# Optimization experiments

Hardware: AMD Instinct MI355X
Metric: run time of the kernel (lower is better)

The kernel has to match this reference:

```python
import jax, jax.numpy as jnp
import numpy as np

B, N, C, H = 4, 1024, 1024, 16
D = C // H                      # head_dim = 64
FFH = int(int(C * 4.0) * 2 / 3) # 2730
EPS = 1e-6


def rmsnorm(x, w):
    return w * (x * jax.lax.rsqrt(jnp.mean(x * x, axis=-1, keepdims=True) + EPS))


def setup_inputs() -> dict:
    key = jax.random.key(0)
    ks = jax.random.split(key, 12)
    s = 0.02
    return {
        "x": jax.random.normal(ks[0], (B, N, C), jnp.float32),
        "c": jax.random.normal(ks[1], (B, C), jnp.float32),
        "norm1_w": jnp.ones((C,), jnp.float32),
        "norm2_w": jnp.ones((C,), jnp.float32),
        "qkv_w": jax.random.normal(ks[2], (3 * C, C), jnp.float32) * s,
        "qkv_b": jnp.zeros((3 * C,), jnp.float32),
        "q_norm_w": jnp.ones((D,), jnp.float32),
        "k_norm_w": jnp.ones((D,), jnp.float32),
        "proj_w": jax.random.normal(ks[3], (C, C), jnp.float32) * s,
        "proj_b": jnp.zeros((C,), jnp.float32),
        "w12_w": jax.random.normal(ks[4], (2 * FFH, C), jnp.float32) * s,
        "w12_b": jnp.zeros((2 * FFH,), jnp.float32),
        "w3_w": jax.random.normal(ks[5], (C, FFH), jnp.float32) * s,
        "w3_b": jnp.zeros((C,), jnp.float32),
        "ada_w": jax.random.normal(ks[6], (6 * C, C), jnp.float32) * s,
        "ada_b": jnp.zeros((6 * C,), jnp.float32),
    }


def modulate(x, shift, scale):
    return x * (1.0 + scale[:, None, :]) + shift[:, None, :]


def attention(x, qkv_w, qkv_b, q_norm_w, k_norm_w, proj_w, proj_b):
    qkv = x @ qkv_w.T + qkv_b                       # (B,N,3C)
    qkv = qkv.reshape(B, N, 3, H, D)
    q, k, v = qkv[:, :, 0], qkv[:, :, 1], qkv[:, :, 2]   # (B,N,H,D)
    q = jnp.transpose(q, (0, 2, 1, 3))              # (B,H,N,D)
    k = jnp.transpose(k, (0, 2, 1, 3))
    v = jnp.transpose(v, (0, 2, 1, 3))
    q = rmsnorm(q, q_norm_w)
    k = rmsnorm(k, k_norm_w)
    attn = jnp.einsum("bhnd,bhmd->bhnm", q, k) / jnp.sqrt(jnp.float32(D))
    attn = jax.nn.softmax(attn, axis=-1)
    out = jnp.einsum("bhnm,bhmd->bhnd", attn, v)
    out = jnp.transpose(out, (0, 2, 1, 3)).reshape(B, N, C)
    return out @ proj_w.T + proj_b


def swiglu(x, w12_w, w12_b, w3_w, w3_b):
    x12 = x @ w12_w.T + w12_b                       # (B,N,2*FFH)
    x1, x2 = x12[..., :FFH], x12[..., FFH:]
    h = jax.nn.silu(x1) * x2
    return h @ w3_w.T + w3_b


def reference(x, c, norm1_w, norm2_w, qkv_w, qkv_b, q_norm_w, k_norm_w,
              proj_w, proj_b, w12_w, w12_b, w3_w, w3_b, ada_w, ada_b):
    ada = jax.nn.silu(c) @ ada_w.T + ada_b          # (B,6C)
    s1, g1, b1, s2, g2, b2 = jnp.split(ada, 6, axis=-1)
    a = attention(modulate(rmsnorm(x, norm1_w), s1, g1),
                  qkv_w, qkv_b, q_norm_w, k_norm_w, proj_w, proj_b)
    x = x + b1[:, None, :] * a
    m = swiglu(modulate(rmsnorm(x, norm2_w), s2, g2), w12_w, w12_b, w3_w, w3_b)
    x = x + b2[:, None, :] * m
    return x
```

## Files before the change

kernel.cpp:

```cpp
#include <hip/hip_runtime.h>

typedef short s16x8 __attribute__((ext_vector_type(8)));
typedef short s16x4 __attribute__((ext_vector_type(4)));
typedef float f32x4 __attribute__((ext_vector_type(4)));

#define B_   4
#define N_   1024
#define C_   1024
#define H_   16
#define D_   64
#define FFH_ 2730
#define FFP_ 2752

__device__ __forceinline__ short f2bf(float f) {
  unsigned u = __float_as_uint(f);
  u += 0x7fff + ((u >> 16) & 1);
  return (short)(unsigned short)(u >> 16);
}
__device__ __forceinline__ float bf2f(short s) {
  return __uint_as_float(((unsigned)(unsigned short)s) << 16);
}
__device__ __forceinline__ float silu(float x) { return x / (1.f + __expf(-x)); }

__device__ __forceinline__ void gload16(const void* g, void* l) {
  __builtin_amdgcn_global_load_lds(
      (const __attribute__((address_space(1))) unsigned*)g,
      (__attribute__((address_space(3))) unsigned*)l, 16, 0, 0);
}

__global__ void cvt3(const float* __restrict__ s0, short* __restrict__ d0, const int n0,
                     const float* __restrict__ s1, short* __restrict__ d1, const int n1,
                     const float* __restrict__ s2, short* __restrict__ d2, const int n2) {
  const int tot = n0 + n1 + n2;
  for (int i = blockIdx.x * 256 + threadIdx.x; i < tot; i += gridDim.x * 256) {
    const float* s; short* d; int j = i;
    if (j < n0)            { s = s0; d = d0; }
    else if ((j -= n0) < n1) { s = s1; d = d1; }
    else                   { j -= n1; s = s2; d = d2; }
    const float4 v = ((const float4*)s)[j];
    s16x4 o;
    o[0] = f2bf(v.x); o[1] = f2bf(v.y); o[2] = f2bf(v.z); o[3] = f2bf(v.w);
    *(s16x4*)(d + (size_t)j * 4) = o;
  }
}

__global__ void cvt_w3(const float* __restrict__ s, short* __restrict__ d) {
  const int col = blockIdx.x * 256 + threadIdx.x;
  const int row = blockIdx.y;
  if (col < FFP_)
    d[(size_t)row * FFP_ + col] = (col < FFH_) ? f2bf(s[(size_t)row * FFH_ + col]) : (short)0;
}

__global__ void ada_gemm(const float* __restrict__ c, const float* __restrict__ aw,
                         const float* __restrict__ ab, float* __restrict__ ada) {
  const int j = blockIdx.x;
  const int l = threadIdx.x;
  float acc[4] = {0.f, 0.f, 0.f, 0.f};
  const float4* wr = (const float4*)(aw + (size_t)j * 1024);
  #pragma unroll
  for (int p = 0; p < 4; ++p) {
    const float4 wv = wr[p * 64 + l];
    #pragma unroll
    for (int b = 0; b < 4; ++b) {
      const float4 cv = ((const float4*)(c + b * 1024))[p * 64 + l];
      acc[b] += silu(cv.x) * wv.x + silu(cv.y) * wv.y + silu(cv.z) * wv.z + silu(cv.w) * wv.w;
    }
  }
  #pragma unroll
  for (int b = 0; b < 4; ++b) {
    float a = acc[b];
    #pragma unroll
    for (int m = 1; m < 64; m <<= 1) a += __shfl_xor(a, m);
    if (l == 0) ada[b * 6144 + j] = a + ab[j];
  }
}

__global__ void rmsmod(const float* __restrict__ x, const float* __restrict__ wn,
                       const float* __restrict__ ada, const int sOff, const int gOff,
                       short* __restrict__ out) {
  const int row = blockIdx.x;
  const int b = row >> 10;
  const int t = threadIdx.x;
  const float4 v = ((const float4*)(x + (size_t)row * 1024))[t];
  float ss = v.x * v.x + v.y * v.y + v.z * v.z + v.w * v.w;
  #pragma unroll
  for (int m = 1; m < 64; m <<= 1) ss += __shfl_xor(ss, m);
  __shared__ float red[4];
  if ((t & 63) == 0) red[t >> 6] = ss;
  __syncthreads();
  const float rs = rsqrtf((red[0] + red[1] + red[2] + red[3]) * (1.f / 1024.f) + 1e-6f);
  const int j = t * 4;
  const float* sp = ada + b * 6144 + sOff + j;
  const float* gp = ada + b * 6144 + gOff + j;
  s16x4 o;
  o[0] = f2bf(v.x * rs * wn[j + 0] * (1.f + gp[0]) + sp[0]);
  o[1] = f2bf(v.y * rs * wn[j + 1] * (1.f + gp[1]) + sp[1]);
  o[2] = f2bf(v.z * rs * wn[j + 2] * (1.f + gp[2]) + sp[2]);
  o[3] = f2bf(v.w * rs * wn[j + 3] * (1.f + gp[3]) + sp[3]);
  *(s16x4*)(out + (size_t)row * 1024 + j) = o;
}

__global__ void rmsmod_b(const short* __restrict__ x, const float* __restrict__ wn,
                         const float* __restrict__ ada, const int sOff, const int gOff,
                         short* __restrict__ out) {
  const int row = blockIdx.x;
  const int b = row >> 10;
  const int t = threadIdx.x;
  const s16x4 vb = *(const s16x4*)(x + (size_t)row * 1024 + t * 4);
  const float v0 = bf2f(vb[0]), v1 = bf2f(vb[1]), v2 = bf2f(vb[2]), v3 = bf2f(vb[3]);
  float ss = v0 * v0 + v1 * v1 + v2 * v2 + v3 * v3;
  #pragma unroll
  for (int m = 1; m < 64; m <<= 1) ss += __shfl_xor(ss, m);
  __shared__ float red[4];
  if ((t & 63) == 0) red[t >> 6] = ss;
  __syncthreads();
  const float rs = rsqrtf((red[0] + red[1] + red[2] + red[3]) * (1.f / 1024.f) + 1e-6f);
  const int j = t * 4;
  const float* sp = ada + b * 6144 + sOff + j;
  const float* gp = ada + b * 6144 + gOff + j;
  s16x4 o;
  o[0] = f2bf(v0 * rs * wn[j + 0] * (1.f + gp[0]) + sp[0]);
  o[1] = f2bf(v1 * rs * wn[j + 1] * (1.f + gp[1]) + sp[1]);
  o[2] = f2bf(v2 * rs * wn[j + 2] * (1.f + gp[2]) + sp[2]);
  o[3] = f2bf(v3 * rs * wn[j + 3] * (1.f + gp[3]) + sp[3]);
  *(s16x4*)(out + (size_t)row * 1024 + j) = o;
}

__launch_bounds__(256, 2)
__global__ void gemm_qkv(const short* __restrict__ A, const short* __restrict__ Bt,
                         const float* __restrict__ bias,
                         short* __restrict__ qbO, short* __restrict__ kbO,
                         short* __restrict__ vrO,
                         const float* __restrict__ qnw, const float* __restrict__ knw) {
  __shared__ short As[128 * 64];
  __shared__ short Bs[128 * 64];
  const int t = threadIdx.x;
  const int l = t & 63;
  const int w = t >> 6;
  const int wr = (w >> 1) * 64, wc = (w & 1) * 64;
  const int K = 1024;

  const int nwg = gridDim.x * gridDim.y;
  int lin = blockIdx.y * gridDim.x + blockIdx.x;
  lin = (lin & 7) * (nwg >> 3) + (lin >> 3);
  const int m0 = (lin / gridDim.x) * 128;
  const int n0 = (lin % gridDim.x) * 128;

  f32x4 acc[4][4];
  const f32x4 z4 = {0.f, 0.f, 0.f, 0.f};
  #pragma unroll
  for (int i = 0; i < 4; ++i)
    #pragma unroll
    for (int j = 0; j < 4; ++j) acc[i][j] = z4;

  const int lr = l >> 3;
  const int lc = (l & 7) ^ lr;
  const short* gAs = A + (size_t)(m0 + w * 32 + lr) * K + lc * 8;
  const short* gBs = Bt + (size_t)(n0 + w * 32 + lr) * K + lc * 8;
  short* lA = As + (w * 32) * 64;
  short* lB = Bs + (w * 32) * 64;

  for (int kt = 0; kt < 16; ++kt) {
    if (kt) __syncthreads();
    const int ko = kt * 64;
    #pragma unroll
    for (int p = 0; p < 4; ++p) {
      gload16(gAs + (size_t)p * 8 * K + ko, lA + p * 8 * 64);
      gload16(gBs + (size_t)p * 8 * K + ko, lB + p * 8 * 64);
    }
    __syncthreads();
    #pragma unroll
    for (int kk = 0; kk < 2; ++kk) {
      const int c16 = kk * 4 + (l >> 4);
      s16x8 af[4], bfr[4];
      #pragma unroll
      for (int mf = 0; mf < 4; ++mf) {
        const int r = wr + mf * 16 + (l & 15);
        af[mf] = *(const s16x8*)&As[r * 64 + ((c16 ^ (r & 7)) << 3)];
      }
      #pragma unroll
      for (int nf = 0; nf < 4; ++nf) {
        const int r = wc + nf * 16 + (l & 15);
        bfr[nf] = *(const s16x8*)&Bs[r * 64 + ((c16 ^ (r & 7)) << 3)];
      }
      __builtin_amdgcn_s_setprio(1);
      #pragma unroll
      for (int mf = 0; mf < 4; ++mf)
        #pragma unroll
        for (int nf = 0; nf < 4; ++nf)
          acc[mf][nf] = __builtin_amdgcn_mfma_f32_16x16x32_bf16(af[mf], bfr[nf], acc[mf][nf], 0, 0, 0);
      __builtin_amdgcn_s_setprio(0);
    }
  }

  const int colB = n0 + wc;
  const int sec = colB >> 10;
  const int hh = (colB >> 6) & 15;
  if (sec < 2) {
    short* dst = sec ? kbO : qbO;
    const float* nw = sec ? knw : qnw;
    const float scl = sec ? 1.f : 0.125f;
    #pragma unroll
    for (int mf = 0; mf < 4; ++mf) {
      #pragma unroll
      for (int i = 0; i < 4; ++i) {
        const int row = m0 + wr + mf * 16 + ((l >> 4) << 2) + i;
        float vv[4];
        float ss = 0.f;
        #pragma unroll
        for (int nf = 0; nf < 4; ++nf) {
          vv[nf] = acc[mf][nf][i] + bias[colB + nf * 16 + (l & 15)];
          ss += vv[nf] * vv[nf];
        }
        ss += __shfl_xor(ss, 1); ss += __shfl_xor(ss, 2);
        ss += __shfl_xor(ss, 4); ss += __shfl_xor(ss, 8);
        const float rs = rsqrtf(ss * (1.f / 64.f) + 1e-6f) * scl;
        const int bb = row >> 10, nn = row & 1023;
        #pragma unroll
        for (int nf = 0; nf < 4; ++nf) {
          const int d = nf * 16 + (l & 15);
          dst[((size_t)(bb * 16 + hh) * 1024 + nn) * 64 + d] = f2bf(vv[nf] * rs * nw[d]);
        }
      }
    }
  } else {
    #pragma unroll
    for (int mf = 0; mf < 4; ++mf)
      #pragma unroll
      for (int nf = 0; nf < 4; ++nf) {
        const int col = colB + nf * 16 + (l & 15);
        const float bsv = bias[col];
        #pragma unroll
        for (int i = 0; i < 4; ++i) {
          const int row = m0 + wr + mf * 16 + ((l >> 4) << 2) + i;
          vrO[(size_t)row * 1024 + (col - 2048)] = f2bf(acc[mf][nf][i] + bsv);
        }
      }
  }
}

template <int MODE>
__launch_bounds__(256, 2)
__global__ void gemm_pw(const short* __restrict__ A, const short* __restrict__ Bt,
                        const int K,
                        const float* __restrict__ bias,
                        const float* __restrict__ adav,
                        const float* __restrict__ residF,
                        const short* __restrict__ residB,
                        void* __restrict__ outP) {
  __shared__ short As[128 * 64];
  __shared__ short Bs[64 * 64];
  const int t = threadIdx.x;
  const int l = t & 63;
  const int w = t >> 6;
  const int wr = (w >> 1) * 64, wc = (w & 1) * 32;

  const int nwg = gridDim.x * gridDim.y;
  int lin = blockIdx.y * gridDim.x + blockIdx.x;
  lin = (lin & 7) * (nwg >> 3) + (lin >> 3);
  const int m0 = (lin / gridDim.x) * 128;
  const int n0 = (lin % gridDim.x) * 64;
  const int nT = K >> 6;

  f32x4 acc[4][2];
  const f32x4 z4 = {0.f, 0.f, 0.f, 0.f};
  #pragma unroll
  for (int i = 0; i < 4; ++i)
    #pragma unroll
    for (int j = 0; j < 2; ++j) acc[i][j] = z4;

  const int lr = l >> 3;
  const int lc = (l & 7) ^ lr;
  const short* gAs = A + (size_t)(m0 + w * 32 + lr) * K + lc * 8;
  const short* gBs = Bt + (size_t)(n0 + w * 16 + lr) * K + lc * 8;
  short* lA = As + (w * 32) * 64;
  short* lB = Bs + (w * 16) * 64;

  for (int kt = 0; kt < nT; ++kt) {
    if (kt) __syncthreads();
    const int ko = kt * 64;
    #pragma unroll
    for (int p = 0; p < 4; ++p)
      gload16(gAs + (size_t)p * 8 * K + ko, lA + p * 8 * 64);
    #pragma unroll
    for (int p = 0; p < 2; ++p)
      gload16(gBs + (size_t)p * 8 * K + ko, lB + p * 8 * 64);
    __syncthreads();
    #pragma unroll
    for (int kk = 0; kk < 2; ++kk) {
      const int c16 = kk * 4 + (l >> 4);
      s16x8 af[4], bfr[2];
      #pragma unroll
      for (int mf = 0; mf < 4; ++mf) {
        const int r = wr + mf * 16 + (l & 15);
        af[mf] = *(const s16x8*)&As[r * 64 + ((c16 ^ (r & 7)) << 3)];
      }
      #pragma unroll
      for (int nf = 0; nf < 2; ++nf) {
        const int r = wc + nf * 16 + (l & 15);
        bfr[nf] = *(const s16x8*)&Bs[r * 64 + ((c16 ^ (r & 7)) << 3)];
      }
      __builtin_amdgcn_s_setprio(1);
      #pragma unroll
      for (int mf = 0; mf < 4; ++mf)
        #pragma unroll
        for (int nf = 0; nf < 2; ++nf)
          acc[mf][nf] = __builtin_amdgcn_mfma_f32_16x16x32_bf16(af[mf], bfr[nf], acc[mf][nf], 0, 0, 0);
      __builtin_amdgcn_s_setprio(0);
    }
  }

  const int bIdx = m0 >> 10;
  #pragma unroll
  for (int mf = 0; mf < 4; ++mf) {
    const int row = m0 + wr + mf * 16 + ((l >> 4) << 2);
    #pragma unroll
    for (int nf = 0; nf < 2; ++nf) {
      const int col = n0 + wc + nf * 16 + (l & 15);
      const float bsv = bias[col];
      const float av = adav[bIdx * 6144 + col];
      #pragma unroll
      for (int i = 0; i < 4; ++i) {
        const float v = acc[mf][nf][i] + bsv;
        const size_t idx = (size_t)(row + i) * 1024 + col;
        if (MODE == 1)
          ((short*)outP)[idx] = f2bf(residF[idx] + av * v);
        else
          ((float*)outP)[idx] = bf2f(residB[idx]) + av * v;
      }
    }
  }
}

__launch_bounds__(256, 2)
__global__ void gemm_w12(const short* __restrict__ A, const short* __restrict__ Bt,
                         const float* __restrict__ bias, short* __restrict__ outH) {
  __shared__ short As[128 * 64];
  __shared__ short B1s[128 * 64];
  __shared__ short B2s[128 * 64];
  const int t = threadIdx.x;
  const int l = t & 63;
  const int w = t >> 6;
  const int wr = (w >> 1) * 64, wc = (w & 1) * 64;

  const int nwg = gridDim.x * gridDim.y;
  int lin = blockIdx.y * gridDim.x + blockIdx.x;
  lin = (lin & 7) * (nwg >> 3) + (lin >> 3);
  const int m0 = (lin / gridDim.x) * 128;
  const int n0 = (lin % gridDim.x) * 128;

  f32x4 a1[4][4], a2[4][4];
  const f32x4 z4 = {0.f, 0.f, 0.f, 0.f};
  #pragma unroll
  for (int i = 0; i < 4; ++i)
    #pragma unroll
    for (int j = 0; j < 4; ++j) { a1[i][j] = z4; a2[i][j] = z4; }

  const int lr = l >> 3;
  const int lc = (l & 7) ^ lr;
  const short* gAs = A + (size_t)(m0 + w * 32 + lr) * 1024 + lc * 8;
  const int rbase = n0 + w * 32 + lr;
  short* lA = As + (w * 32) * 64;
  short* lB1 = B1s + (w * 32) * 64;
  short* lB2 = B2s + (w * 32) * 64;

  for (int kt = 0; kt < 16; ++kt) {
    if (kt) __syncthreads();
    const int ko = kt * 64;
    #pragma unroll
    for (int p = 0; p < 4; ++p) {
      int j = rbase + p * 8;
      if (j >= FFH_) j = FFH_ - 1;
      gload16(gAs + (size_t)p * 8 * 1024 + ko, lA + p * 8 * 64);
      gload16(Bt + (size_t)j * 1024 + ko + lc * 8, lB1 + p * 8 * 64);
      gload16(Bt + (size_t)(j + FFH_) * 1024 + ko + lc * 8, lB2 + p * 8 * 64);
    }
    __syncthreads();
    #pragma unroll
    for (int kk = 0; kk < 2; ++kk) {
      const int c16 = kk * 4 + (l >> 4);
      s16x8 af[4], b1f[4], b2f[4];
      #pragma unroll
      for (int mf = 0; mf < 4; ++mf) {
        const int r = wr + mf * 16 + (l & 15);
        af[mf] = *(const s16x8*)&As[r * 64 + ((c16 ^ (r & 7)) << 3)];
      }
      #pragma unroll
      for (int nf = 0; nf < 4; ++nf) {
        const int r = wc + nf * 16 + (l & 15);
        const int idx = r * 64 + ((c16 ^ (r & 7)) << 3);
        b1f[nf] = *(const s16x8*)&B1s[idx];
        b2f[nf] = *(const s16x8*)&B2s[idx];
      }
      __builtin_amdgcn_s_setprio(1);
      #pragma unroll
      for (int mf = 0; mf < 4; ++mf)
        #pragma unroll
        for (int nf = 0; nf < 4; ++nf) {
          a1[mf][nf] = __builtin_amdgcn_mfma_f32_16x16x32_bf16(af[mf], b1f[nf], a1[mf][nf], 0, 0, 0);
          a2[mf][nf] = __builtin_amdgcn_mfma_f32_16x16x32_bf16(af[mf], b2f[nf], a2[mf][nf], 0, 0, 0);
        }
      __builtin_amdgcn_s_setprio(0);
    }
  }

  #pragma unroll
  for (int mf = 0; mf < 4; ++mf) {
    const int row = m0 + wr + mf * 16 + ((l >> 4) << 2);
    #pragma unroll
    for (int nf = 0; nf < 4; ++nf) {
      const int col = n0 + wc + nf * 16 + (l & 15);
      if (col < FFP_) {
        const bool real = col < FFH_;
        const float bb1 = real ? bias[col] : 0.f;
        const float bb2 = real ? bias[col + FFH_] : 0.f;
        #pragma unroll
        for (int i = 0; i < 4; ++i) {
          float o = 0.f;
          if (real) {
            const float v1 = a1[mf][nf][i] + bb1;
            const float v2 = a2[mf][nf][i] + bb2;
            o = silu(v1) * v2;
          }
          outH[(size_t)(row + i) * FFP_ + col] = f2bf(o);
        }
      }
    }
  }
}

__global__ void v_trans(const short* __restrict__ vr, short* __restrict__ vt) {
  __shared__ short ld[64][72];
  const int t = threadIdx.x;
  const int bh = blockIdx.y, b = bh >> 4, h = bh & 15;
  const int n0 = blockIdx.x * 64;
  const int nl = t >> 2, cb = (t & 3) * 16;
  const short* src = vr + (size_t)(b * 1024 + n0 + nl) * 1024 + h * 64 + cb;
  *(s16x8*)&ld[nl][cb] = *(const s16x8*)src;
  *(s16x8*)&ld[nl][cb + 8] = *(const s16x8*)(src + 8);
  __syncthreads();
  const int d = t >> 2, np = (t & 3) * 16;
  short* dst = vt + (size_t)(bh * 64 + d) * 1024 + n0 + np;
  s16x8 o0, o1;
  #pragma unroll
  for (int p = 0; p < 8; ++p) { o0[p] = ld[np + p][d]; o1[p] = ld[np + 8 + p][d]; }
  *(s16x8*)dst = o0;
  *(s16x8*)(dst + 8) = o1;
}

__launch_bounds__(256, 2)
__global__ void attn(const short* __restrict__ qb, const short* __restrict__ kb,
                     const short* __restrict__ vt, short* __restrict__ ob) {
  __shared__ short Ks[64 * 64];
  __shared__ short Vs[64 * 64];
  __shared__ short Pl[4][32 * 64];
  const int t = threadIdx.x, l = t & 63, w = t >> 6;
  const int bh = blockIdx.y, b = bh >> 4, h = bh & 15;
  const int q0 = blockIdx.x * 128 + w * 32;
  const short* qp = qb + (size_t)bh * (N_ * D_);
  const short* kp = kb + (size_t)bh * (N_ * D_);
  const short* vp = vt + (size_t)bh * (D_ * N_);

  s16x8 qf[2][2];
  #pragma unroll
  for (int mf = 0; mf < 2; ++mf)
    #pragma unroll
    for (int kk = 0; kk < 2; ++kk)
      qf[mf][kk] = *(const s16x8*)&qp[(q0 + mf * 16 + (l & 15)) * 64 + kk * 32 + ((l >> 4) * 8)];

  f32x4 aco[2][4];
  float rm[2][4], rl[2][4];
  const f32x4 z4 = {0.f, 0.f, 0.f, 0.f};
  #pragma unroll
  for (int mf = 0; mf < 2; ++mf) {
    #pragma unroll
    for (int nd = 0; nd < 4; ++nd) aco[mf][nd] = z4;
    #pragma unroll
    for (int i = 0; i < 4; ++i) { rm[mf][i] = -1e30f; rl[mf][i] = 0.f; }
  }

  const int sr = t >> 2, sc = (t & 3) * 2;
  s16x8 rk[2], rv[2];
  #pragma unroll
  for (int p = 0; p < 2; ++p) {
    rk[p] = *(const s16x8*)&kp[sr * 64 + (sc + p) * 8];
    rv[p] = *(const s16x8*)&vp[sr * 1024 + (sc + p) * 8];
  }

  for (int kt = 0; kt < 16; ++kt) {
    if (kt) __syncthreads();
    #pragma unroll
    for (int p = 0; p < 2; ++p) {
      const int cs = ((sc + p) ^ (sr & 7)) << 3;
      *(s16x8*)&Ks[sr * 64 + cs] = rk[p];
      *(s16x8*)&Vs[sr * 64 + cs] = rv[p];
    }
    __syncthreads();
    if (kt < 15) {
      const int kv0 = (kt + 1) * 64;
      #pragma unroll
      for (int p = 0; p < 2; ++p) {
        rk[p] = *(const s16x8*)&kp[(kv0 + sr) * 64 + (sc + p) * 8];
        rv[p] = *(const s16x8*)&vp[sr * 1024 + kv0 + (sc + p) * 8];
      }
    }

    f32x4 s[2][4];
    #pragma unroll
    for (int mf = 0; mf < 2; ++mf)
      #pragma unroll
      for (int nf = 0; nf < 4; ++nf) s[mf][nf] = z4;

    #pragma unroll
    for (int kk = 0; kk < 2; ++kk) {
      const int c16 = kk * 4 + (l >> 4);
      s16x8 kf[4];
      #pragma unroll
      for (int nf = 0; nf < 4; ++nf) {
        const int r = nf * 16 + (l & 15);
        kf[nf] = *(const s16x8*)&Ks[r * 64 + ((c16 ^ (r & 7)) << 3)];
      }
      __builtin_amdgcn_s_setprio(1);
      #pragma unroll
      for (int mf = 0; mf < 2; ++mf)
        #pragma unroll
        for (int nf = 0; nf < 4; ++nf)
          s[mf][nf] = __builtin_amdgcn_mfma_f32_16x16x32_bf16(qf[mf][kk], kf[nf], s[mf][nf], 0, 0, 0);
      __builtin_amdgcn_s_setprio(0);
    }

    #pragma unroll
    for (int mf = 0; mf < 2; ++mf) {
      #pragma unroll
      for (int i = 0; i < 4; ++i) {
        float pm = fmaxf(fmaxf(s[mf][0][i], s[mf][1][i]), fmaxf(s[mf][2][i], s[mf][3][i]));
        pm = fmaxf(pm, __shfl_xor(pm, 1));
        pm = fmaxf(pm, __shfl_xor(pm, 2));
        pm = fmaxf(pm, __shfl_xor(pm, 4));
        pm = fmaxf(pm, __shfl_xor(pm, 8));
        const float nm = fmaxf(rm[mf][i], pm);
        const float corr = __expf(rm[mf][i] - nm);
        rm[mf][i] = nm;
        float rs = 0.f;
        #pragma unroll
        for (int nf = 0; nf < 4; ++nf) {
          const float p = __expf(s[mf][nf][i] - nm);
          s[mf][nf][i] = p;
          rs += p;
        }
        rs += __shfl_xor(rs, 1);
        rs += __shfl_xor(rs, 2);
        rs += __shfl_xor(rs, 4);
        rs += __shfl_xor(rs, 8);
        rl[mf][i] = rl[mf][i] * corr + rs;
        #pragma unroll
        for (int nd = 0; nd < 4; ++nd) aco[mf][nd][i] *= corr;
      }
    }

    short* pw = &Pl[w][0];
    #pragma unroll
    for (int mf = 0; mf < 2; ++mf)
      #pragma unroll
      for (int nf = 0; nf < 4; ++nf)
        #pragma unroll
        for (int i = 0; i < 4; ++i) {
          const int row = mf * 16 + ((l >> 4) << 2) + i;
          const int col = nf * 16 + (l & 15);
          pw[row * 64 + (((col >> 3) ^ (row & 7)) << 3) + (col & 7)] = f2bf(s[mf][nf][i]);
        }

    #pragma unroll
    for (int kk = 0; kk < 2; ++kk) {
      const int c16 = kk * 4 + (l >> 4);
      s16x8 vf[4];
      #pragma unroll
      for (int nd = 0; nd < 4; ++nd) {
        const int r = nd * 16 + (l & 15);
        vf[nd] = *(const s16x8*)&Vs[r * 64 + ((c16 ^ (r & 7)) << 3)];
      }
      __builtin_amdgcn_s_setprio(1);
      #pragma unroll
      for (int mf = 0; mf < 2; ++mf) {
        const int pr = mf * 16 + (l & 15);
        const s16x8 pf = *(const s16x8*)&pw[pr * 64 + ((c16 ^ (pr & 7)) << 3)];
        #pragma unroll
        for (int nd = 0; nd < 4; ++nd)
          aco[mf][nd] = __builtin_amdgcn_mfma_f32_16x16x32_bf16(pf, vf[nd], aco[mf][nd], 0, 0, 0);
      }
      __builtin_amdgcn_s_setprio(0);
    }
  }

  #pragma unroll
  for (int mf = 0; mf < 2; ++mf)
    #pragma unroll
    for (int i = 0; i < 4; ++i) {
      const float inv = 1.f / rl[mf][i];
      const int row = q0 + mf * 16 + ((l >> 4) << 2) + i;
      #pragma unroll
      for (int nd = 0; nd < 4; ++nd) {
        const int col = h * 64 + nd * 16 + (l & 15);
        ob[(size_t)(b * 1024 + row) * 1024 + col] = f2bf(aco[mf][nd][i] * inv);
      }
    }
}

extern "C" void kernel_launch(void* const* d_in, const int* in_sizes, int n_in,
                              void* d_out, int out_size, void* d_ws, size_t ws_size,
                              hipStream_t stream) {
  const float* x     = (const float*)d_in[0];
  const float* c     = (const float*)d_in[1];
  const float* n1w   = (const float*)d_in[2];
  const float* n2w   = (const float*)d_in[3];
  const float* qkvw  = (const float*)d_in[4];
  const float* qkvb  = (const float*)d_in[5];
  const float* qnw   = (const float*)d_in[6];
  const float* knw   = (const float*)d_in[7];
  const float* projw = (const float*)d_in[8];
  const float* projb = (const float*)d_in[9];
  const float* w12w  = (const float*)d_in[10];
  const float* w12b  = (const float*)d_in[11];
  const float* w3w   = (const float*)d_in[12];
  const float* w3b   = (const float*)d_in[13];
  const float* adaw  = (const float*)d_in[14];
  const float* adab  = (const float*)d_in[15];
  float* outp = (float*)d_out;

  char* ws = (char*)d_ws;
  size_t off = 0;
  auto alloc = [&](size_t bytes) { void* p = ws + off; off += (bytes + 255) & ~(size_t)255; return p; };
  short* WQKV = (short*)alloc(3072ull * 1024 * 2);
  short* WPROJ = (short*)alloc(1024ull * 1024 * 2);
  short* W12B = (short*)alloc(5460ull * 1024 * 2);
  short* W3B  = (short*)alloc(1024ull * FFP_ * 2);
  float* ADA  = (float*)alloc(4ull * 6144 * 4);
  short* H1   = (short*)alloc(4096ull * 1024 * 2);
  short* QBF  = (short*)alloc(64ull * 1024 * 64 * 2);
  short* KBF  = (short*)alloc(64ull * 1024 * 64 * 2);
  short* VROW = (short*)alloc(4096ull * 1024 * 2);
  short* VTB  = (short*)alloc(64ull * 64 * 1024 * 2);
  short* OBF  = (short*)alloc(4096ull * 1024 * 2);
  short* X1B  = (short*)alloc(4096ull * 1024 * 2);
  short* H2   = (short*)alloc(4096ull * 1024 * 2);
  short* HB   = (short*)alloc(4096ull * FFP_ * 2);

  cvt3<<<2048, 256, 0, stream>>>(qkvw, WQKV, 3072 * 1024 / 4,
                                 projw, WPROJ, 1024 * 1024 / 4,
                                 w12w, W12B, 5460 * 1024 / 4);
  cvt_w3<<<dim3(11, 1024), 256, 0, stream>>>(w3w, W3B);
  ada_gemm<<<6144, 64, 0, stream>>>(c, adaw, adab, ADA);
  rmsmod<<<4096, 256, 0, stream>>>(x, n1w, ADA, 0, 1024, H1);
  gemm_qkv<<<dim3(24, 32), 256, 0, stream>>>(H1, WQKV, qkvb, QBF, KBF, VROW, qnw, knw);
  v_trans<<<dim3(16, 64), 256, 0, stream>>>(VROW, VTB);
  attn<<<dim3(8, 64), 256, 0, stream>>>(QBF, KBF, VTB, OBF);
  gemm_pw<1><<<dim3(16, 32), 256, 0, stream>>>(OBF, WPROJ, 1024, projb,
      ADA + 2048, x, nullptr, X1B);
  rmsmod_b<<<4096, 256, 0, stream>>>(X1B, n2w, ADA, 3072, 4096, H2);
  gemm_w12<<<dim3(22, 32), 256, 0, stream>>>(H2, W12B, w12b, HB);
  gemm_pw<4><<<dim3(16, 32), 256, 0, stream>>>(HB, W3B, FFP_, w3b,
      ADA + 5120, nullptr, X1B, outp);
}
```

Baseline: 262.4 us.

## Triple-buffer LDS with async global_load_lds prefetch in projection and W12 GEMMs

Replaces the load-then-sync single-buffer main loops of gemm_pw and gemm_w12 with a three-stage LDS ring. Global-to-LDS loads run two k-tiles ahead and are gated with explicit vmcnt waits plus raw barriers, so memory latency overlaps with MFMA work. gemm_w12 also halves its k-tile to 32 so the three stages fit in LDS, which needs a new swizzle and addressing scheme. The cost is more LDS per block (possible occupancy loss), more loop iterations in w12, and correctness that depends on hand-counted vmcnt values.

```diff
diff --git a/kernel.cpp b/kernel.cpp
--- a/kernel.cpp
+++ b/kernel.cpp
@@ -27,6 +27,14 @@
       (const __attribute__((address_space(1))) unsigned*)g,
       (__attribute__((address_space(3))) unsigned*)l, 16, 0, 0);
 }
+
+#define GATE3(more2, more1)                                                    \
+  do {                                                                         \
+    if (more2)      asm volatile("s_waitcnt vmcnt(12)" ::: "memory");          \
+    else if (more1) asm volatile("s_waitcnt vmcnt(6)" ::: "memory");           \
+    else            asm volatile("s_waitcnt vmcnt(0)" ::: "memory");           \
+    __builtin_amdgcn_s_barrier();                                              \
+  } while (0)
 
 __global__ void cvt3(const float* __restrict__ s0, short* __restrict__ d0, const int n0,
                      const float* __restrict__ s1, short* __restrict__ d1, const int n1,
@@ -248,8 +256,8 @@
                         const float* __restrict__ residF,
                         const short* __restrict__ residB,
                         void* __restrict__ outP) {
-  __shared__ short As[128 * 64];
-  __shared__ short Bs[64 * 64];
+  __shared__ short As[3][128 * 64];
+  __shared__ short Bs[3][64 * 64];
   const int t = threadIdx.x;
   const int l = t & 63;
   const int w = t >> 6;
@@ -273,19 +281,23 @@
   const int lc = (l & 7) ^ lr;
   const short* gAs = A + (size_t)(m0 + w * 32 + lr) * K + lc * 8;
   const short* gBs = Bt + (size_t)(n0 + w * 16 + lr) * K + lc * 8;
-  short* lA = As + (w * 32) * 64;
-  short* lB = Bs + (w * 16) * 64;
-
+
+#define STGP(s, kt)                                                            \
+  do {                                                                         \
+    const int _ko = (kt) * 64;                                                 \
+    _Pragma("unroll") for (int p = 0; p < 4; ++p)                              \
+      gload16(gAs + (size_t)p * 8 * K + _ko, &As[s][(w * 32 + p * 8) * 64]);   \
+    _Pragma("unroll") for (int p = 0; p < 2; ++p)                              \
+      gload16(gBs + (size_t)p * 8 * K + _ko, &Bs[s][(w * 16 + p * 8) * 64]);   \
+  } while (0)
+
+  STGP(0, 0);
+  if (nT > 1) STGP(1, 1);
+
+  int cur = 0, s2 = 2;
   for (int kt = 0; kt < nT; ++kt) {
-    if (kt) __syncthreads();
-    const int ko = kt * 64;
-    #pragma unroll
-    for (int p = 0; p < 4; ++p)
-      gload16(gAs + (size_t)p * 8 * K + ko, lA + p * 8 * 64);
-    #pragma unroll
-    for (int p = 0; p < 2; ++p)
-      gload16(gBs + (size_t)p * 8 * K + ko, lB + p * 8 * 64);
-    __syncthreads();
+    if (kt + 2 < nT) STGP(s2, kt + 2);
+    GATE3(kt + 2 < nT, kt + 1 < nT);
     #pragma unroll
     for (int kk = 0; kk < 2; ++kk) {
       const int c16 = kk * 4 + (l >> 4);
@@ -293,12 +305,12 @@
       #pragma unroll
       for (int mf = 0; mf < 4; ++mf) {
         const int r = wr + mf * 16 + (l & 15);
-        af[mf] = *(const s16x8*)&As[r * 64 + ((c16 ^ (r & 7)) << 3)];
+        af[mf] = *(const s16x8*)&As[cur][r * 64 + ((c16 ^ (r & 7)) << 3)];
       }
       #pragma unroll
       for (int nf = 0; nf < 2; ++nf) {
         const int r = wc + nf * 16 + (l & 15);
-        bfr[nf] = *(const s16x8*)&Bs[r * 64 + ((c16 ^ (r & 7)) << 3)];
+        bfr[nf] = *(const s16x8*)&Bs[cur][r * 64 + ((c16 ^ (r & 7)) << 3)];
       }
       __builtin_amdgcn_s_setprio(1);
       #pragma unroll
@@ -308,7 +320,11 @@
           acc[mf][nf] = __builtin_amdgcn_mfma_f32_16x16x32_bf16(af[mf], bfr[nf], acc[mf][nf], 0, 0, 0);
       __builtin_amdgcn_s_setprio(0);
     }
-  }
+    __builtin_amdgcn_s_barrier();
+    cur = (cur == 2) ? 0 : cur + 1;
+    s2 = (s2 == 2) ? 0 : s2 + 1;
+  }
+#undef STGP
 
   const int bIdx = m0 >> 10;
   #pragma unroll
@@ -335,9 +351,9 @@
 __launch_bounds__(256, 2)
 __global__ void gemm_w12(const short* __restrict__ A, const short* __restrict__ Bt,
                          const float* __restrict__ bias, short* __restrict__ outH) {
-  __shared__ short As[128 * 64];
-  __shared__ short B1s[128 * 64];
-  __shared__ short B2s[128 * 64];
+  __shared__ short As[3][128 * 32];
+  __shared__ short B1s[3][128 * 32];
+  __shared__ short B2s[3][128 * 32];
   const int t = threadIdx.x;
   const int l = t & 63;
   const int w = t >> 6;
@@ -356,53 +372,63 @@
     #pragma unroll
     for (int j = 0; j < 4; ++j) { a1[i][j] = z4; a2[i][j] = z4; }
 
-  const int lr = l >> 3;
-  const int lc = (l & 7) ^ lr;
-  const short* gAs = A + (size_t)(m0 + w * 32 + lr) * 1024 + lc * 8;
-  const int rbase = n0 + w * 32 + lr;
-  short* lA = As + (w * 32) * 64;
-  short* lB1 = B1s + (w * 32) * 64;
-  short* lB2 = B2s + (w * 32) * 64;
-
-  for (int kt = 0; kt < 16; ++kt) {
-    if (kt) __syncthreads();
-    const int ko = kt * 64;
-    #pragma unroll
-    for (int p = 0; p < 4; ++p) {
-      int j = rbase + p * 8;
-      if (j >= FFH_) j = FFH_ - 1;
-      gload16(gAs + (size_t)p * 8 * 1024 + ko, lA + p * 8 * 64);
-      gload16(Bt + (size_t)j * 1024 + ko + lc * 8, lB1 + p * 8 * 64);
-      gload16(Bt + (size_t)(j + FFH_) * 1024 + ko + lc * 8, lB2 + p * 8 * 64);
-    }
-    __syncthreads();
-    #pragma unroll
-    for (int kk = 0; kk < 2; ++kk) {
-      const int c16 = kk * 4 + (l >> 4);
-      s16x8 af[4], b1f[4], b2f[4];
-      #pragma unroll
-      for (int mf = 0; mf < 4; ++mf) {
-        const int r = wr + mf * 16 + (l & 15);
-        af[mf] = *(const s16x8*)&As[r * 64 + ((c16 ^ (r & 7)) << 3)];
-      }
+  const int srow = l >> 2;
+  const int schk = (l & 3) ^ (srow & 3);
+  const short* gA0 = A + (size_t)(m0 + w * 32 + srow) * 1024 + schk * 8;
+  const short* gA1 = A + (size_t)(m0 + w * 32 + 16 + srow) * 1024 + schk * 8;
+  int j0 = n0 + w * 32 + srow;      if (j0 >= FFH_) j0 = FFH_ - 1;
+  int j1 = n0 + w * 32 + 16 + srow; if (j1 >= FFH_) j1 = FFH_ - 1;
+  const short* gB10 = Bt + (size_t)j0 * 1024 + schk * 8;
+  const short* gB11 = Bt + (size_t)j1 * 1024 + schk * 8;
+  const short* gB20 = Bt + (size_t)(j0 + FFH_) * 1024 + schk * 8;
+  const short* gB21 = Bt + (size_t)(j1 + FFH_) * 1024 + schk * 8;
+
+#define STGW(s, kt)                                                            \
+  do {                                                                         \
+    const int _ko = (kt) * 32;                                                 \
+    gload16(gA0 + _ko,  &As[s][(w * 2 + 0) * 512]);                            \
+    gload16(gA1 + _ko,  &As[s][(w * 2 + 1) * 512]);                            \
+    gload16(gB10 + _ko, &B1s[s][(w * 2 + 0) * 512]);                           \
+    gload16(gB11 + _ko, &B1s[s][(w * 2 + 1) * 512]);                           \
+    gload16(gB20 + _ko, &B2s[s][(w * 2 + 0) * 512]);                           \
+    gload16(gB21 + _ko, &B2s[s][(w * 2 + 1) * 512]);                           \
+  } while (0)
+
+  STGW(0, 0);
+  STGW(1, 1);
+
+  const int fr = l & 15;
+  const int rofs = fr * 32 + (((l >> 4) ^ (fr & 3)) << 3);
+  const int ga = (w >> 1) * 4;
+  const int gb = (w & 1) * 4;
+
+  int cur = 0, s2 = 2;
+  for (int kt = 0; kt < 32; ++kt) {
+    if (kt + 2 < 32) STGW(s2, kt + 2);
+    GATE3(kt + 2 < 32, kt + 1 < 32);
+    s16x8 af[4], b1f[4], b2f[4];
+    #pragma unroll
+    for (int mf = 0; mf < 4; ++mf)
+      af[mf] = *(const s16x8*)&As[cur][(ga + mf) * 512 + rofs];
+    #pragma unroll
+    for (int nf = 0; nf < 4; ++nf) {
+      b1f[nf] = *(const s16x8*)&B1s[cur][(gb + nf) * 512 + rofs];
+      b2f[nf] = *(const s16x8*)&B2s[cur][(gb + nf) * 512 + rofs];
+    }
+    __builtin_amdgcn_s_setprio(1);
+    #pragma unroll
+    for (int mf = 0; mf < 4; ++mf)
       #pragma unroll
       for (int nf = 0; nf < 4; ++nf) {
-        const int r = wc + nf * 16 + (l & 15);
-        const int idx = r * 64 + ((c16 ^ (r & 7)) << 3);
-        b1f[nf] = *(const s16x8*)&B1s[idx];
-        b2f[nf] = *(const s16x8*)&B2s[idx];
-      }
-      __builtin_amdgcn_s_setprio(1);
-      #pragma unroll
-      for (int mf = 0; mf < 4; ++mf)
-        #pragma unroll
-        for (int nf = 0; nf < 4; ++nf) {
-          a1[mf][nf] = __builtin_amdgcn_mfma_f32_16x16x32_bf16(af[mf], b1f[nf], a1[mf][nf], 0, 0, 0);
-          a2[mf][nf] = __builtin_amdgcn_mfma_f32_16x16x32_bf16(af[mf], b2f[nf], a2[mf][nf], 0, 0, 0);
-        }
-      __builtin_amdgcn_s_setprio(0);
-    }
-  }
+        a1[mf][nf] = __builtin_amdgcn_mfma_f32_16x16x32_bf16(af[mf], b1f[nf], a1[mf][nf], 0, 0, 0);
+        a2[mf][nf] = __builtin_amdgcn_mfma_f32_16x16x32_bf16(af[mf], b2f[nf], a2[mf][nf], 0, 0, 0);
+      }
+    __builtin_amdgcn_s_setprio(0);
+    __builtin_amdgcn_s_barrier();
+    cur = (cur == 2) ? 0 : cur + 1;
+    s2 = (s2 == 2) ? 0 : s2 + 1;
+  }
+#undef STGW
 
   #pragma unroll
   for (int mf = 0; mf < 4; ++mf) {
```

After: 275.7 us. 1.05x slower.
